# Performance work log

Measured on AMD Instinct MI355X. Metric: run time of the kernel, lower is better.

The kernel has to match this reference:

```python
import jax, jax.numpy as jnp
import numpy as np

NUM_LAYERS = 2
FEATURES = 128
INPUT_SIZE = 128
HIDDEN = 512
BATCH = 128
SEQ_LEN = 512
PRED_LEN = 128


def _uniform(key, shape, fan):
    bound = 1.0 / np.sqrt(fan)
    return jax.random.uniform(key, shape, jnp.float32, -bound, bound)


def setup_inputs() -> dict:
    key = jax.random.key(0)
    ks = jax.random.split(key, 14)
    inp = {}
    inp["x"] = jax.random.normal(ks[0], (BATCH, SEQ_LEN, FEATURES), jnp.float32)
    # encoder Linear(features -> input_size)
    inp["enc_w"] = _uniform(ks[1], (INPUT_SIZE, FEATURES), FEATURES)
    inp["enc_b"] = _uniform(ks[2], (INPUT_SIZE,), FEATURES)
    # decoder Linear(hidden -> input_size)
    inp["dec_w"] = _uniform(ks[3], (INPUT_SIZE, HIDDEN), HIDDEN)
    inp["dec_b"] = _uniform(ks[4], (INPUT_SIZE,), HIDDEN)
    # LSTM layer 0 (input_size -> hidden), gate order i,f,g,o as in PyTorch
    inp["wih0"] = _uniform(ks[5], (4 * HIDDEN, INPUT_SIZE), HIDDEN)
    inp["whh0"] = _uniform(ks[6], (4 * HIDDEN, HIDDEN), HIDDEN)
    inp["bih0"] = _uniform(ks[7], (4 * HIDDEN,), HIDDEN)
    inp["bhh0"] = _uniform(ks[8], (4 * HIDDEN,), HIDDEN)
    # LSTM layer 1 (hidden -> hidden)
    inp["wih1"] = _uniform(ks[9], (4 * HIDDEN, HIDDEN), HIDDEN)
    inp["whh1"] = _uniform(ks[10], (4 * HIDDEN, HIDDEN), HIDDEN)
    inp["bih1"] = _uniform(ks[11], (4 * HIDDEN,), HIDDEN)
    inp["bhh1"] = _uniform(ks[12], (4 * HIDDEN,), HIDDEN)
    inp["pred_len"] = PRED_LEN
    return inp


def _lstm_cell(h, c, inp, wih, whh, bih, bhh):
    g = inp @ wih.T + bih + h @ whh.T + bhh  # [B, 4H]
    i, f, gg, o = jnp.split(g, 4, axis=-1)
    c = jax.nn.sigmoid(f) * c + jax.nn.sigmoid(i) * jnp.tanh(gg)
    h = jax.nn.sigmoid(o) * jnp.tanh(c)
    return h, c


def reference(x, enc_w, enc_b, dec_w, dec_b, wih0, whh0, bih0, bhh0,
              wih1, whh1, bih1, bhh1, pred_len):
    B, S, Fdim = x.shape
    T = S + pred_len - 1
    # pad x to T steps; beyond S the input comes from the previous output
    x_pad = jnp.concatenate([x, jnp.zeros((B, pred_len - 1, Fdim), x.dtype)], axis=1)
    x_t = jnp.transpose(x_pad, (1, 0, 2))  # [T, B, F]

    def step(carry, xs):
        h0, c0, h1, c1, prev_out = carry
        xt, t = xs
        inp = jnp.where(t < S, xt, prev_out)
        e = inp @ enc_w.T + enc_b                    # encoder
        h0, c0 = _lstm_cell(h0, c0, e, wih0, whh0, bih0, bhh0)
        h1, c1 = _lstm_cell(h1, c1, h0, wih1, whh1, bih1, bhh1)
        out = h1 @ dec_w.T + dec_b                   # decoder
        return (h0, c0, h1, c1, out), out

    z = jnp.zeros((B, HIDDEN), x.dtype)
    init = (z, z, z, z, jnp.zeros((B, Fdim), x.dtype))
    _, outs = jax.lax.scan(step, init, (x_t, jnp.arange(T)))
    # keep steps idx >= S-1 (pred_len outputs), back to [B, pred_len, input_size]
    return jnp.transpose(outs[S - 1:], (1, 0, 2))
```

## Files before the change

### kernel.cpp

```cpp
#include <hip/hip_runtime.h>
#include <math.h>

#define HID 512
#define FEAT 128
#define SEQL 512
#define PREDL 128
#define NWG 256
#define HK 516
#define EK 132

typedef float v2f __attribute__((ext_vector_type(2)));

__device__ __forceinline__ float sigf_(float x) { return 1.0f / (1.0f + __expf(-x)); }
__device__ __forceinline__ float tanh_(float x) {
  float ax = fabsf(x);
  float e2 = __expf(-2.0f * ax);
  return copysignf((1.0f - e2) / (1.0f + e2), x);
}

__device__ __forceinline__ void stg_sc(float* p, float v) {
  __hip_atomic_store(p, v, __ATOMIC_RELAXED, __HIP_MEMORY_SCOPE_AGENT);
}

__device__ __forceinline__ void bar_arrive(int* __restrict__ bar, int grp,
                                           int phase, int tid, bool& last) {
  __syncthreads();
  if (tid == 0) {
    const int a = __hip_atomic_fetch_add(bar + grp * 32, 1, __ATOMIC_RELAXED,
                                         __HIP_MEMORY_SCOPE_AGENT);
    last = (a == 32 * phase - 1);
    if (last)
      __hip_atomic_store(bar + 512 + grp * 32, phase, __ATOMIC_RELAXED,
                         __HIP_MEMORY_SCOPE_AGENT);
  }
  asm volatile("" ::: "memory");
}
__device__ __forceinline__ void bar_wait(int* __restrict__ bar, int grp,
                                         int phase, int tid, bool last) {
  asm volatile("" ::: "memory");
  if (tid == 0 && !last) {
    while (__hip_atomic_load(bar + 512 + grp * 32, __ATOMIC_RELAXED,
                             __HIP_MEMORY_SCOPE_AGENT) < phase)
      __builtin_amdgcn_s_sleep(1);
  }
  __syncthreads();
}

__device__ __forceinline__ void stage_h2(float* __restrict__ dA,
                                         const float* __restrict__ sA,
                                         float* __restrict__ dB,
                                         const float* __restrict__ sB,
                                         int b0, int tid) {
  const int kb = tid >> 2;
  const int bq = (tid & 3) * 4;
  const float* a0 = sA + (size_t)kb * 128 + b0 + bq;
  const float* a1 = sA + ((size_t)kb + 128) * 128 + b0 + bq;
  const float* a2 = sA + ((size_t)kb + 256) * 128 + b0 + bq;
  const float* a3 = sA + ((size_t)kb + 384) * 128 + b0 + bq;
  const float* c0 = sB + (size_t)kb * 128 + b0 + bq;
  const float* c1 = sB + ((size_t)kb + 128) * 128 + b0 + bq;
  const float* c2 = sB + ((size_t)kb + 256) * 128 + b0 + bq;
  const float* c3 = sB + ((size_t)kb + 384) * 128 + b0 + bq;
  float4 r0, r1, r2, r3, q0, q1, q2, q3;
  asm volatile(
      "global_load_dwordx4 %0, %8, off sc0 sc1\n\t"
      "global_load_dwordx4 %1, %9, off sc0 sc1\n\t"
      "global_load_dwordx4 %2, %10, off sc0 sc1\n\t"
      "global_load_dwordx4 %3, %11, off sc0 sc1\n\t"
      "global_load_dwordx4 %4, %12, off sc0 sc1\n\t"
      "global_load_dwordx4 %5, %13, off sc0 sc1\n\t"
      "global_load_dwordx4 %6, %14, off sc0 sc1\n\t"
      "global_load_dwordx4 %7, %15, off sc0 sc1\n\t"
      "s_waitcnt vmcnt(0)"
      : "=&v"(r0), "=&v"(r1), "=&v"(r2), "=&v"(r3),
        "=&v"(q0), "=&v"(q1), "=&v"(q2), "=&v"(q3)
      : "v"(a0), "v"(a1), "v"(a2), "v"(a3),
        "v"(c0), "v"(c1), "v"(c2), "v"(c3)
      : "memory");
  dA[(bq + 0) * HK + kb] = r0.x; dA[(bq + 1) * HK + kb] = r0.y;
  dA[(bq + 2) * HK + kb] = r0.z; dA[(bq + 3) * HK + kb] = r0.w;
  dA[(bq + 0) * HK + kb + 128] = r1.x; dA[(bq + 1) * HK + kb + 128] = r1.y;
  dA[(bq + 2) * HK + kb + 128] = r1.z; dA[(bq + 3) * HK + kb + 128] = r1.w;
  dA[(bq + 0) * HK + kb + 256] = r2.x; dA[(bq + 1) * HK + kb + 256] = r2.y;
  dA[(bq + 2) * HK + kb + 256] = r2.z; dA[(bq + 3) * HK + kb + 256] = r2.w;
  dA[(bq + 0) * HK + kb + 384] = r3.x; dA[(bq + 1) * HK + kb + 384] = r3.y;
  dA[(bq + 2) * HK + kb + 384] = r3.z; dA[(bq + 3) * HK + kb + 384] = r3.w;
  dB[(bq + 0) * HK + kb] = q0.x; dB[(bq + 1) * HK + kb] = q0.y;
  dB[(bq + 2) * HK + kb] = q0.z; dB[(bq + 3) * HK + kb] = q0.w;
  dB[(bq + 0) * HK + kb + 128] = q1.x; dB[(bq + 1) * HK + kb + 128] = q1.y;
  dB[(bq + 2) * HK + kb + 128] = q1.z; dB[(bq + 3) * HK + kb + 128] = q1.w;
  dB[(bq + 0) * HK + kb + 256] = q2.x; dB[(bq + 1) * HK + kb + 256] = q2.y;
  dB[(bq + 2) * HK + kb + 256] = q2.z; dB[(bq + 3) * HK + kb + 256] = q2.w;
  dB[(bq + 0) * HK + kb + 384] = q3.x; dB[(bq + 1) * HK + kb + 384] = q3.y;
  dB[(bq + 2) * HK + kb + 384] = q3.z; dB[(bq + 3) * HK + kb + 384] = q3.w;
}
__device__ __forceinline__ void stage_h1t(float* __restrict__ dst,
                                          const float* __restrict__ src,
                                          int b0, int tid) {
  const int kb = tid >> 2;
  const int bq = (tid & 3) * 4;
  const float* p0 = src + (size_t)kb * 128 + b0 + bq;
  const float* p1 = src + ((size_t)kb + 128) * 128 + b0 + bq;
  const float* p2 = src + ((size_t)kb + 256) * 128 + b0 + bq;
  const float* p3 = src + ((size_t)kb + 384) * 128 + b0 + bq;
  float4 r0, r1, r2, r3;
  asm volatile(
      "global_load_dwordx4 %0, %4, off sc0 sc1\n\t"
      "global_load_dwordx4 %1, %5, off sc0 sc1\n\t"
      "global_load_dwordx4 %2, %6, off sc0 sc1\n\t"
      "global_load_dwordx4 %3, %7, off sc0 sc1\n\t"
      "s_waitcnt vmcnt(0)"
      : "=&v"(r0), "=&v"(r1), "=&v"(r2), "=&v"(r3)
      : "v"(p0), "v"(p1), "v"(p2), "v"(p3)
      : "memory");
  dst[(bq + 0) * HK + kb] = r0.x; dst[(bq + 1) * HK + kb] = r0.y;
  dst[(bq + 2) * HK + kb] = r0.z; dst[(bq + 3) * HK + kb] = r0.w;
  dst[(bq + 0) * HK + kb + 128] = r1.x; dst[(bq + 1) * HK + kb + 128] = r1.y;
  dst[(bq + 2) * HK + kb + 128] = r1.z; dst[(bq + 3) * HK + kb + 128] = r1.w;
  dst[(bq + 0) * HK + kb + 256] = r2.x; dst[(bq + 1) * HK + kb + 256] = r2.y;
  dst[(bq + 2) * HK + kb + 256] = r2.z; dst[(bq + 3) * HK + kb + 256] = r2.w;
  dst[(bq + 0) * HK + kb + 384] = r3.x; dst[(bq + 1) * HK + kb + 384] = r3.y;
  dst[(bq + 2) * HK + kb + 384] = r3.z; dst[(bq + 3) * HK + kb + 384] = r3.w;
}
__device__ __forceinline__ void stage_x(float* __restrict__ dst,
                                        const float* __restrict__ x, int t,
                                        int b0, int tid) {
  const int bb = tid >> 5;
  const int fq = (tid & 31) * 4;
  const float4 v =
      *(const float4*)(x + ((size_t)(b0 + bb) * SEQL + t) * FEAT + fq);
  *(float4*)(dst + bb * EK + fq) = v;
}

__device__ __forceinline__ void pkf(v2f& a01, v2f& a23, float4 w, float h) {
  v2f hh; hh[0] = h; hh[1] = h;
  v2f lo; lo[0] = w.x; lo[1] = w.y;
  v2f hi; hi[0] = w.z; hi[1] = w.w;
  a01 = __builtin_elementwise_fma(lo, hh, a01);
  a23 = __builtin_elementwise_fma(hi, hh, a23);
}
__device__ __forceinline__ void gemv_fused8(v2f& a01, v2f& a23,
                                            const float4* __restrict__ W8,
                                            size_t base,
                                            const float* __restrict__ rA,
                                            const float* __restrict__ rB,
                                            int k4b, int k4e) {
#pragma unroll 2
  for (int k4 = k4b; k4 < k4e; ++k4) {
    const float4 hA = *(const float4*)(rA + k4 * 4);
    const float4 hB = *(const float4*)(rB + k4 * 4);
    const size_t o = base + (size_t)k4 * 8;
    pkf(a01, a23, W8[o + 0], hA.x); pkf(a01, a23, W8[o + 1], hB.x);
    pkf(a01, a23, W8[o + 2], hA.y); pkf(a01, a23, W8[o + 3], hB.y);
    pkf(a01, a23, W8[o + 4], hA.z); pkf(a01, a23, W8[o + 5], hB.z);
    pkf(a01, a23, W8[o + 6], hA.w); pkf(a01, a23, W8[o + 7], hB.w);
  }
}
__device__ __forceinline__ void gemv_half8(v2f& a01, v2f& a23,
                                           const float4* __restrict__ W8,
                                           size_t base, int sel,
                                           const float* __restrict__ row,
                                           int nk4) {
#pragma unroll 4
  for (int k4 = 0; k4 < nk4; ++k4) {
    const float4 h = *(const float4*)(row + k4 * 4);
    const size_t o = base + (size_t)k4 * 8 + sel;
    pkf(a01, a23, W8[o + 0], h.x);
    pkf(a01, a23, W8[o + 2], h.y);
    pkf(a01, a23, W8[o + 4], h.z);
    pkf(a01, a23, W8[o + 6], h.w);
  }
}
__device__ __forceinline__ void gemv_p4(v2f& a01, v2f& a23,
                                        const float4* __restrict__ W4,
                                        size_t base,
                                        const float* __restrict__ row,
                                        int nk4) {
#pragma unroll 4
  for (int k4 = 0; k4 < nk4; ++k4) {
    const float4 h = *(const float4*)(row + k4 * 4);
    const size_t o = base + (size_t)k4 * 4;
    pkf(a01, a23, W4[o + 0], h.x);
    pkf(a01, a23, W4[o + 1], h.y);
    pkf(a01, a23, W4[o + 2], h.z);
    pkf(a01, a23, W4[o + 3], h.w);
  }
}

__device__ __forceinline__ void act_store(v2f a01, v2f a23, float& c_reg,
                                          float* __restrict__ HoutT,
                                          size_t cit) {
  const float ig = sigf_(a01[0]), fg = sigf_(a01[1]);
  const float gg = tanh_(a23[0]), og = sigf_(a23[1]);
  const float cn = fg * c_reg + ig * gg;
  c_reg = cn;
  stg_sc(HoutT + cit, og * tanh_(cn));
}

__global__ __launch_bounds__(512, 1) void k_persist(
    const float* __restrict__ x,
    const float* __restrict__ enc4, const float* __restrict__ enc_b,
    const float* __restrict__ wih04, const float* __restrict__ Wa8,
    const float* __restrict__ Wf8,
    const float* __restrict__ bih0, const float* __restrict__ bhh0,
    const float* __restrict__ bih1, const float* __restrict__ bhh1,
    const float* __restrict__ dec_w, const float* __restrict__ dec_b,
    const float* __restrict__ bcomp,
    float* __restrict__ h0A, float* __restrict__ h0B,
    float* __restrict__ h1A, float* __restrict__ h1B,
    int* __restrict__ bar, float* __restrict__ out) {
  __shared__ float s_h0[16 * HK];
  __shared__ float s_h1[16 * HK];
  __shared__ float s_x[16 * EK];
  __shared__ float s_e[16 * EK];
  __shared__ float s_red[1536];

  const int wg = blockIdx.x;
  const int tid = threadIdx.x;
  const int ut = (wg & 7) * 4 + ((wg >> 3) & 3);
  const int bt = wg >> 5;
  const int b0 = bt * 16;
  const int t8 = tid & 255;
  const int u = t8 >> 4, b = t8 & 15;
  const int ug = ut * 16 + u;
  const size_t cit = (size_t)ug * 128 + b0 + b;

  float* h0b[2] = {h0A, h0B};
  float* h1b[2] = {h1A, h1B};
  const float* sh0row = s_h0 + b * HK;
  const float* sh1row = s_h1 + b * HK;
  const float* serow = s_e + b * EK;

  const float4* W8a = (const float4*)Wa8;
  const float4* W8f = (const float4*)Wf8;
  const float4* W4i = (const float4*)wih04;
  const float4* W4e = (const float4*)enc4;
  const size_t baseG = (size_t)ug * 1024;
  const size_t baseI = (size_t)ug * 128;

  const float bt00 = bih0[ug] + bhh0[ug];
  const float bt01 = bih0[512 + ug] + bhh0[512 + ug];
  const float bt02 = bih0[1024 + ug] + bhh0[1024 + ug];
  const float bt03 = bih0[1536 + ug] + bhh0[1536 + ug];
  const float ba00 = bt00 + bcomp[ug];
  const float ba01 = bt01 + bcomp[512 + ug];
  const float ba02 = bt02 + bcomp[1024 + ug];
  const float ba03 = bt03 + bcomp[1536 + ug];
  const float b10 = bih1[ug] + bhh1[ug];
  const float b11 = bih1[512 + ug] + bhh1[512 + ug];
  const float b12 = bih1[1024 + ug] + bhh1[1024 + ug];
  const float b13 = bih1[1536 + ug] + bhh1[1536 + ug];

  const int eb = tid & 15;
  const int fb = tid >> 4;
  const size_t baseE = (size_t)fb * 128;
  const float eb0 = enc_b[fb * 4], eb1 = enc_b[fb * 4 + 1];
  const float eb2 = enc_b[fb * 4 + 2], eb3 = enc_b[fb * 4 + 3];
  const float* sxrow = s_x + eb * EK;

  const int djj = tid >> 7, dbb = (tid >> 3) & 15, dk8 = tid & 7;
  const int jd = (wg & 31) * 4 + djj;
  const float4* decr = (const float4*)(dec_w + (size_t)jd * HID);
  const float* dhrow = s_h1 + dbb * HK;

  float c_reg = 0.0f;
  int ph = 0;
  bool last = false;

  stage_x(s_x, x, 0, b0, tid);
  for (int t = 0; t < SEQL; ++t) {
    const float* h0in = h0b[(t + 1) & 1];
    float* h0out = h0b[t & 1];
    const float* h1in = h1b[t & 1];
    float* h1out = h1b[(t + 1) & 1];

    stage_h2(s_h0, h0in, s_h1, h1in, b0, tid);
    __syncthreads();

    {
      v2f a01; a01[0] = eb0; a01[1] = eb1;
      v2f a23; a23[0] = eb2; a23[1] = eb3;
      gemv_p4(a01, a23, W4e, baseE, sxrow, 32);
      *(float4*)(s_e + eb * EK + fb * 4) =
          make_float4(a01[0], a01[1], a23[0], a23[1]);
    }
    __syncthreads();

    if (tid < 256) {
      v2f a01; a01[0] = bt00; a01[1] = bt01;
      v2f a23; a23[0] = bt02; a23[1] = bt03;
      gemv_half8(a01, a23, W8a, baseG, 1, sh0row, 128);
      gemv_p4(a01, a23, W4i, baseI, serow, 32);
      act_store(a01, a23, c_reg, h0out, cit);
    } else if (t > 0) {
      v2f a01; a01[0] = b10; a01[1] = b11;
      v2f a23; a23[0] = b12; a23[1] = b13;
      gemv_fused8(a01, a23, W8f, baseG, sh0row, sh1row, 0, 128);
      act_store(a01, a23, c_reg, h1out, cit);
    }
    bar_arrive(bar, bt, ++ph, tid, last);
    if (t + 1 < SEQL) stage_x(s_x, x, t + 1, b0, tid);
    bar_wait(bar, bt, ph, tid, last);
  }

  stage_h2(s_h0, h0b[1], s_h1, h1b[0], b0, tid);
  __syncthreads();
  {
    const int own = (tid >= 256);
    v2f a01, a23;
    if (own) { a01[0] = b10; a01[1] = b11; a23[0] = b12; a23[1] = b13; }
    else { a01[0] = 0; a01[1] = 0; a23[0] = 0; a23[1] = 0; }
    const int kb4 = own ? 0 : 64;
    gemv_fused8(a01, a23, W8f, baseG, sh0row, sh1row, kb4, kb4 + 64);
    if (!own) {
      *(float4*)(s_red + t8 * 4) = make_float4(a01[0], a01[1], a23[0], a23[1]);
    }
    __syncthreads();
    if (own) {
      const float4 p = *(const float4*)(s_red + t8 * 4);
      a01[0] += p.x; a01[1] += p.y; a23[0] += p.z; a23[1] += p.w;
      act_store(a01, a23, c_reg, h1b[1], cit);
    }
  }
  bar_arrive(bar, bt, ++ph, tid, last);
  bar_wait(bar, bt, ph, tid, last);

  for (int t = SEQL; t < SEQL + PREDL - 1; ++t) {
    const float* h1prev = h1b[(t + 1) & 1];
    const float* h0prev = h0b[(t + 1) & 1];
    float* h0cur = h0b[t & 1];
    float* h1cur = h1b[t & 1];

    stage_h2(s_h1, h1prev, s_h0, h0prev, b0, tid);
    __syncthreads();
    {
      const int own = (tid < 256);
      v2f a01, a23;
      if (own) { a01[0] = ba00; a01[1] = ba01; a23[0] = ba02; a23[1] = ba03; }
      else { a01[0] = 0; a01[1] = 0; a23[0] = 0; a23[1] = 0; }
      const int kb4 = own ? 0 : 64;
      gemv_fused8(a01, a23, W8a, baseG, sh1row, sh0row, kb4, kb4 + 64);
      float dacc = 0.0f;
#pragma unroll 4
      for (int k4 = dk8 * 16; k4 < dk8 * 16 + 16; ++k4) {
        const float4 w = decr[k4];
        const float4 h = *(const float4*)(dhrow + k4 * 4);
        dacc += w.x * h.x + w.y * h.y + w.z * h.z + w.w * h.w;
      }
      s_red[1024 + tid] = dacc;
      if (!own)
        *(float4*)(s_red + t8 * 4) = make_float4(a01[0], a01[1], a23[0], a23[1]);
      __syncthreads();
      if (own) {
        const float4 p = *(const float4*)(s_red + t8 * 4);
        a01[0] += p.x; a01[1] += p.y; a23[0] += p.z; a23[1] += p.w;
        act_store(a01, a23, c_reg, h0cur, cit);
      }
      if (dk8 == 0) {
        float s = dec_b[jd];
#pragma unroll
        for (int i = 0; i < 8; ++i) s += s_red[1024 + tid + i];
        out[((size_t)(b0 + dbb) * PREDL + (t - SEQL)) * FEAT + jd] = s;
      }
    }
    bar_arrive(bar, bt, ++ph, tid, last);
    bar_wait(bar, bt, ph, tid, last);

    stage_h1t(s_h0, h0cur, b0, tid);
    __syncthreads();
    {
      const int own = (tid >= 256);
      v2f a01, a23;
      if (own) { a01[0] = b10; a01[1] = b11; a23[0] = b12; a23[1] = b13; }
      else { a01[0] = 0; a01[1] = 0; a23[0] = 0; a23[1] = 0; }
      const int kb4 = own ? 0 : 64;
      gemv_fused8(a01, a23, W8f, baseG, sh0row, sh1row, kb4, kb4 + 64);
      if (!own)
        *(float4*)(s_red + t8 * 4) = make_float4(a01[0], a01[1], a23[0], a23[1]);
      __syncthreads();
      if (own) {
        const float4 p = *(const float4*)(s_red + t8 * 4);
        a01[0] += p.x; a01[1] += p.y; a23[0] += p.z; a23[1] += p.w;
        act_store(a01, a23, c_reg, h1cur, cit);
      }
    }
    bar_arrive(bar, bt, ++ph, tid, last);
    bar_wait(bar, bt, ph, tid, last);
  }

  stage_h1t(s_h1, h1b[0], b0, tid);
  __syncthreads();
  {
    float dacc = 0.0f;
#pragma unroll 4
    for (int k4 = dk8 * 16; k4 < dk8 * 16 + 16; ++k4) {
      const float4 w = decr[k4];
      const float4 h = *(const float4*)(dhrow + k4 * 4);
      dacc += w.x * h.x + w.y * h.y + w.z * h.z + w.w * h.w;
    }
    s_red[1024 + tid] = dacc;
    __syncthreads();
    if (dk8 == 0) {
      float s = dec_b[jd];
#pragma unroll
      for (int i = 0; i < 8; ++i) s += s_red[1024 + tid + i];
      out[((size_t)(b0 + dbb) * PREDL + (PREDL - 1)) * FEAT + jd] = s;
    }
  }
}

__global__ void k_b1(const float* __restrict__ enc_w,
                     const float* __restrict__ dec_w, float* __restrict__ B1) {
  const int idx = blockIdx.x * 256 + threadIdx.x;
  const int j = idx >> 9, m = idx & 511;
  float acc = 0.0f;
  for (int k = 0; k < FEAT; ++k) acc += enc_w[j * FEAT + k] * dec_w[k * HID + m];
  B1[idx] = acc;
}
__global__ void k_te(const float* __restrict__ enc_w,
                     const float* __restrict__ enc_b,
                     const float* __restrict__ dec_b, float* __restrict__ te) {
  const int j = threadIdx.x;
  float acc = enc_b[j];
  for (int k = 0; k < FEAT; ++k) acc += dec_b[k] * enc_w[j * FEAT + k];
  te[j] = acc;
}
__global__ void k_bcomp(const float* __restrict__ wih0,
                        const float* __restrict__ te, float* __restrict__ bc) {
  const int n = blockIdx.x * 256 + threadIdx.x;
  float acc = 0.0f;
  for (int j = 0; j < FEAT; ++j) acc += wih0[n * FEAT + j] * te[j];
  bc[n] = acc;
}
__global__ void k_wa8(const float* __restrict__ wih0,
                      const float* __restrict__ B1,
                      const float* __restrict__ whh0, float* __restrict__ W) {
  const int idx = blockIdx.x * 256 + threadIdx.x;
  const int uu = idx >> 9, k = idx & 511;
  float c[4];
#pragma unroll
  for (int g = 0; g < 4; ++g) {
    const float* wr = wih0 + ((size_t)(g * 512 + uu)) * FEAT;
    float acc = 0.0f;
    for (int j = 0; j < FEAT; ++j) acc += wr[j] * B1[j * HID + k];
    c[g] = acc;
  }
  float4* o = (float4*)(W + ((size_t)(uu * 512 + k)) * 8);
  o[0] = make_float4(c[0], c[1], c[2], c[3]);
  o[1] = make_float4(whh0[((size_t)uu) * 512 + k],
                     whh0[((size_t)(512 + uu)) * 512 + k],
                     whh0[((size_t)(1024 + uu)) * 512 + k],
                     whh0[((size_t)(1536 + uu)) * 512 + k]);
}
__global__ void k_wf8(const float* __restrict__ wih1,
                      const float* __restrict__ whh1, float* __restrict__ W) {
  const int idx = blockIdx.x * 256 + threadIdx.x;
  const int uu = idx >> 9, k = idx & 511;
  float4* o = (float4*)(W + ((size_t)(uu * 512 + k)) * 8);
  o[0] = make_float4(wih1[((size_t)uu) * 512 + k],
                     wih1[((size_t)(512 + uu)) * 512 + k],
                     wih1[((size_t)(1024 + uu)) * 512 + k],
                     wih1[((size_t)(1536 + uu)) * 512 + k]);
  o[1] = make_float4(whh1[((size_t)uu) * 512 + k],
                     whh1[((size_t)(512 + uu)) * 512 + k],
                     whh1[((size_t)(1024 + uu)) * 512 + k],
                     whh1[((size_t)(1536 + uu)) * 512 + k]);
}
__global__ void k_wih04(const float* __restrict__ wih0, float* __restrict__ W) {
  const int idx = blockIdx.x * 256 + threadIdx.x;
  const int uu = idx >> 7, k = idx & 127;
  float4* o = (float4*)(W + ((size_t)idx) * 4);
  o[0] = make_float4(wih0[((size_t)uu) * FEAT + k],
                     wih0[((size_t)(512 + uu)) * FEAT + k],
                     wih0[((size_t)(1024 + uu)) * FEAT + k],
                     wih0[((size_t)(1536 + uu)) * FEAT + k]);
}
__global__ void k_enc4(const float* __restrict__ enc_w, float* __restrict__ W) {
  const int idx = blockIdx.x * 256 + threadIdx.x;
  const int fb = idx >> 7, k = idx & 127;
  float4* o = (float4*)(W + ((size_t)idx) * 4);
  o[0] = make_float4(enc_w[((size_t)(fb * 4 + 0)) * FEAT + k],
                     enc_w[((size_t)(fb * 4 + 1)) * FEAT + k],
                     enc_w[((size_t)(fb * 4 + 2)) * FEAT + k],
                     enc_w[((size_t)(fb * 4 + 3)) * FEAT + k]);
}

#define WS_H0A 0
#define WS_H0B 65536
#define WS_H1A 131072
#define WS_H1B 196608
#define WS_BAR 262144
#define WS_B1 263168
#define WS_TE 328704
#define WS_BCOMP 328832
#define WS_WIH04 330880
#define WS_ENC4 593024
#define WS_WA8 609408
#define WS_WF8 2706560

extern "C" void kernel_launch(void* const* d_in, const int* in_sizes, int n_in,
                              void* d_out, int out_size, void* d_ws,
                              size_t ws_size, hipStream_t stream) {
  const float* x     = (const float*)d_in[0];
  const float* enc_w = (const float*)d_in[1];
  const float* enc_b = (const float*)d_in[2];
  const float* dec_w = (const float*)d_in[3];
  const float* dec_b = (const float*)d_in[4];
  const float* wih0  = (const float*)d_in[5];
  const float* whh0  = (const float*)d_in[6];
  const float* bih0  = (const float*)d_in[7];
  const float* bhh0  = (const float*)d_in[8];
  const float* wih1  = (const float*)d_in[9];
  const float* whh1  = (const float*)d_in[10];
  const float* bih1  = (const float*)d_in[11];
  const float* bhh1  = (const float*)d_in[12];
  float* out = (float*)d_out;

  float* ws = (float*)d_ws;
  float* h0A = ws + WS_H0A;
  float* h0B = ws + WS_H0B;
  float* h1A = ws + WS_H1A;
  float* h1B = ws + WS_H1B;
  int* bar = (int*)(ws + WS_BAR);
  float* B1 = ws + WS_B1;
  float* te = ws + WS_TE;
  float* bcomp = ws + WS_BCOMP;
  float* wih04 = ws + WS_WIH04;
  float* enc4 = ws + WS_ENC4;
  float* Wa8 = ws + WS_WA8;
  float* Wf8 = ws + WS_WF8;

  hipMemsetAsync(ws, 0, (size_t)WS_B1 * sizeof(float), stream);

  k_b1<<<256, 256, 0, stream>>>(enc_w, dec_w, B1);
  k_te<<<1, 128, 0, stream>>>(enc_w, enc_b, dec_b, te);
  k_bcomp<<<8, 256, 0, stream>>>(wih0, te, bcomp);
  k_wa8<<<1024, 256, 0, stream>>>(wih0, B1, whh0, Wa8);
  k_wf8<<<1024, 256, 0, stream>>>(wih1, whh1, Wf8);
  k_wih04<<<256, 256, 0, stream>>>(wih0, wih04);
  k_enc4<<<16, 256, 0, stream>>>(enc_w, enc4);

  k_persist<<<NWG, 512, 0, stream>>>(
      x, enc4, enc_b, wih04, Wa8, Wf8, bih0, bhh0, bih1, bhh1,
      dec_w, dec_b, bcomp, h0A, h0B, h1A, h1B, bar, out);
}
```

Baseline: 37.38 ms.

## Double persistent workgroup to 1024 threads with split-K GEMV crews

Raises the persistent kernel from 512 to 1024 threads per workgroup and splits each gate GEMV's K range across two thread halves, reducing the partial sums through shared memory. Layer-1 tail steps use a four-way K split, and the decoder moves to its own thread crew with a repacked float4 weight layout so it runs alongside the layer-0 update. The encoder is re-tiled to two outputs per thread. The intent is to shorten the latency of each serial time step. In exchange it adds an extra __syncthreads per step, higher register pressure at 1024 threads, and shared-memory reductions.

```diff
diff --git a/kernel.cpp b/kernel.cpp
--- a/kernel.cpp
+++ b/kernel.cpp
@@ -17,6 +17,7 @@
   float e2 = __expf(-2.0f * ax);
   return copysignf((1.0f - e2) / (1.0f + e2), x);
 }
+__device__ __forceinline__ v2f mkv2(float a, float b) { v2f r; r[0] = a; r[1] = b; return r; }
 
 __device__ __forceinline__ void stg_sc(float* p, float v) {
   __hip_atomic_store(p, v, __ATOMIC_RELAXED, __HIP_MEMORY_SCOPE_AGENT);
@@ -46,59 +47,11 @@
   __syncthreads();
 }
 
-__device__ __forceinline__ void stage_h2(float* __restrict__ dA,
-                                         const float* __restrict__ sA,
-                                         float* __restrict__ dB,
-                                         const float* __restrict__ sB,
-                                         int b0, int tid) {
-  const int kb = tid >> 2;
-  const int bq = (tid & 3) * 4;
-  const float* a0 = sA + (size_t)kb * 128 + b0 + bq;
-  const float* a1 = sA + ((size_t)kb + 128) * 128 + b0 + bq;
-  const float* a2 = sA + ((size_t)kb + 256) * 128 + b0 + bq;
-  const float* a3 = sA + ((size_t)kb + 384) * 128 + b0 + bq;
-  const float* c0 = sB + (size_t)kb * 128 + b0 + bq;
-  const float* c1 = sB + ((size_t)kb + 128) * 128 + b0 + bq;
-  const float* c2 = sB + ((size_t)kb + 256) * 128 + b0 + bq;
-  const float* c3 = sB + ((size_t)kb + 384) * 128 + b0 + bq;
-  float4 r0, r1, r2, r3, q0, q1, q2, q3;
-  asm volatile(
-      "global_load_dwordx4 %0, %8, off sc0 sc1\n\t"
-      "global_load_dwordx4 %1, %9, off sc0 sc1\n\t"
-      "global_load_dwordx4 %2, %10, off sc0 sc1\n\t"
-      "global_load_dwordx4 %3, %11, off sc0 sc1\n\t"
-      "global_load_dwordx4 %4, %12, off sc0 sc1\n\t"
-      "global_load_dwordx4 %5, %13, off sc0 sc1\n\t"
-      "global_load_dwordx4 %6, %14, off sc0 sc1\n\t"
-      "global_load_dwordx4 %7, %15, off sc0 sc1\n\t"
-      "s_waitcnt vmcnt(0)"
-      : "=&v"(r0), "=&v"(r1), "=&v"(r2), "=&v"(r3),
-        "=&v"(q0), "=&v"(q1), "=&v"(q2), "=&v"(q3)
-      : "v"(a0), "v"(a1), "v"(a2), "v"(a3),
-        "v"(c0), "v"(c1), "v"(c2), "v"(c3)
-      : "memory");
-  dA[(bq + 0) * HK + kb] = r0.x; dA[(bq + 1) * HK + kb] = r0.y;
-  dA[(bq + 2) * HK + kb] = r0.z; dA[(bq + 3) * HK + kb] = r0.w;
-  dA[(bq + 0) * HK + kb + 128] = r1.x; dA[(bq + 1) * HK + kb + 128] = r1.y;
-  dA[(bq + 2) * HK + kb + 128] = r1.z; dA[(bq + 3) * HK + kb + 128] = r1.w;
-  dA[(bq + 0) * HK + kb + 256] = r2.x; dA[(bq + 1) * HK + kb + 256] = r2.y;
-  dA[(bq + 2) * HK + kb + 256] = r2.z; dA[(bq + 3) * HK + kb + 256] = r2.w;
-  dA[(bq + 0) * HK + kb + 384] = r3.x; dA[(bq + 1) * HK + kb + 384] = r3.y;
-  dA[(bq + 2) * HK + kb + 384] = r3.z; dA[(bq + 3) * HK + kb + 384] = r3.w;
-  dB[(bq + 0) * HK + kb] = q0.x; dB[(bq + 1) * HK + kb] = q0.y;
-  dB[(bq + 2) * HK + kb] = q0.z; dB[(bq + 3) * HK + kb] = q0.w;
-  dB[(bq + 0) * HK + kb + 128] = q1.x; dB[(bq + 1) * HK + kb + 128] = q1.y;
-  dB[(bq + 2) * HK + kb + 128] = q1.z; dB[(bq + 3) * HK + kb + 128] = q1.w;
-  dB[(bq + 0) * HK + kb + 256] = q2.x; dB[(bq + 1) * HK + kb + 256] = q2.y;
-  dB[(bq + 2) * HK + kb + 256] = q2.z; dB[(bq + 3) * HK + kb + 256] = q2.w;
-  dB[(bq + 0) * HK + kb + 384] = q3.x; dB[(bq + 1) * HK + kb + 384] = q3.y;
-  dB[(bq + 2) * HK + kb + 384] = q3.z; dB[(bq + 3) * HK + kb + 384] = q3.w;
-}
-__device__ __forceinline__ void stage_h1t(float* __restrict__ dst,
-                                          const float* __restrict__ src,
-                                          int b0, int tid) {
-  const int kb = tid >> 2;
-  const int bq = (tid & 3) * 4;
+__device__ __forceinline__ void stage4(float* __restrict__ dst,
+                                       const float* __restrict__ src,
+                                       int b0, int lane512) {
+  const int kb = lane512 >> 2;
+  const int bq = (lane512 & 3) * 4;
   const float* p0 = src + (size_t)kb * 128 + b0 + bq;
   const float* p1 = src + ((size_t)kb + 128) * 128 + b0 + bq;
   const float* p2 = src + ((size_t)kb + 256) * 128 + b0 + bq;
@@ -122,11 +75,11 @@
   dst[(bq + 0) * HK + kb + 384] = r3.x; dst[(bq + 1) * HK + kb + 384] = r3.y;
   dst[(bq + 2) * HK + kb + 384] = r3.z; dst[(bq + 3) * HK + kb + 384] = r3.w;
 }
-__device__ __forceinline__ void stage_x(float* __restrict__ dst,
-                                        const float* __restrict__ x, int t,
-                                        int b0, int tid) {
-  const int bb = tid >> 5;
-  const int fq = (tid & 31) * 4;
+__device__ __forceinline__ void stage_x1(float* __restrict__ dst,
+                                         const float* __restrict__ x, int t,
+                                         int b0, int lane512) {
+  const int bb = lane512 >> 5;
+  const int fq = (lane512 & 31) * 4;
   const float4 v =
       *(const float4*)(x + ((size_t)(b0 + bb) * SEQL + t) * FEAT + fq);
   *(float4*)(dst + bb * EK + fq) = v;
@@ -160,9 +113,9 @@
                                            const float4* __restrict__ W8,
                                            size_t base, int sel,
                                            const float* __restrict__ row,
-                                           int nk4) {
+                                           int k4b, int k4e) {
 #pragma unroll 4
-  for (int k4 = 0; k4 < nk4; ++k4) {
+  for (int k4 = k4b; k4 < k4e; ++k4) {
     const float4 h = *(const float4*)(row + k4 * 4);
     const size_t o = base + (size_t)k4 * 8 + sel;
     pkf(a01, a23, W8[o + 0], h.x);
@@ -175,9 +128,9 @@
                                         const float4* __restrict__ W4,
                                         size_t base,
                                         const float* __restrict__ row,
-                                        int nk4) {
+                                        int k4b, int k4e) {
 #pragma unroll 4
-  for (int k4 = 0; k4 < nk4; ++k4) {
+  for (int k4 = k4b; k4 < k4e; ++k4) {
     const float4 h = *(const float4*)(row + k4 * 4);
     const size_t o = base + (size_t)k4 * 4;
     pkf(a01, a23, W4[o + 0], h.x);
@@ -197,14 +150,14 @@
   stg_sc(HoutT + cit, og * tanh_(cn));
 }
 
-__global__ __launch_bounds__(512, 1) void k_persist(
+__global__ __launch_bounds__(1024, 1) void k_persist(
     const float* __restrict__ x,
-    const float* __restrict__ enc4, const float* __restrict__ enc_b,
+    const float* __restrict__ enc2, const float* __restrict__ enc_b,
     const float* __restrict__ wih04, const float* __restrict__ Wa8,
     const float* __restrict__ Wf8,
     const float* __restrict__ bih0, const float* __restrict__ bhh0,
     const float* __restrict__ bih1, const float* __restrict__ bhh1,
-    const float* __restrict__ dec_w, const float* __restrict__ dec_b,
+    const float* __restrict__ dec4, const float* __restrict__ dec_b,
     const float* __restrict__ bcomp,
     float* __restrict__ h0A, float* __restrict__ h0B,
     float* __restrict__ h1A, float* __restrict__ h1B,
@@ -213,17 +166,21 @@
   __shared__ float s_h1[16 * HK];
   __shared__ float s_x[16 * EK];
   __shared__ float s_e[16 * EK];
-  __shared__ float s_red[1536];
+  __shared__ float4 s_red4[768];
 
   const int wg = blockIdx.x;
   const int tid = threadIdx.x;
   const int ut = (wg & 7) * 4 + ((wg >> 3) & 3);
   const int bt = wg >> 5;
   const int b0 = bt * 16;
-  const int t8 = tid & 255;
-  const int u = t8 >> 4, b = t8 & 15;
+  const int o = tid & 255;
+  const int u = o >> 4, b = o & 15;
   const int ug = ut * 16 + u;
   const size_t cit = (size_t)ug * 128 + b0 + b;
+  const int crewB = tid >> 9;
+  const int khalf = (tid >> 8) & 1;
+  const int lane512 = tid & 511;
+  const int q4 = ((tid >> 8) + 2) & 3;
 
   float* h0b[2] = {h0A, h0B};
   float* h1b[2] = {h1A, h1B};
@@ -234,7 +191,6 @@
   const float4* W8a = (const float4*)Wa8;
   const float4* W8f = (const float4*)Wf8;
   const float4* W4i = (const float4*)wih04;
-  const float4* W4e = (const float4*)enc4;
   const size_t baseG = (size_t)ug * 1024;
   const size_t baseI = (size_t)ug * 128;
 
@@ -252,78 +208,100 @@
   const float b13 = bih1[1536 + ug] + bhh1[1536 + ug];
 
   const int eb = tid & 15;
-  const int fb = tid >> 4;
-  const size_t baseE = (size_t)fb * 128;
-  const float eb0 = enc_b[fb * 4], eb1 = enc_b[fb * 4 + 1];
-  const float eb2 = enc_b[fb * 4 + 2], eb3 = enc_b[fb * 4 + 3];
+  const int f2 = tid >> 4;
+  const float4* EF4 = (const float4*)enc2 + (size_t)f2 * 64;
+  const float encb0 = enc_b[f2 * 2], encb1 = enc_b[f2 * 2 + 1];
   const float* sxrow = s_x + eb * EK;
 
-  const int djj = tid >> 7, dbb = (tid >> 3) & 15, dk8 = tid & 7;
-  const int jd = (wg & 31) * 4 + djj;
-  const float4* decr = (const float4*)(dec_w + (size_t)jd * HID);
-  const float* dhrow = s_h1 + dbb * HK;
+  const int cb = tid & 511;
+  const int jq = cb >> 4, db = cb & 15;
+  const float4* D4 = (const float4*)dec4;
+  const size_t baseD = (size_t)jq * 512;
+  const float db0 = dec_b[jq * 4], db1 = dec_b[jq * 4 + 1];
+  const float db2 = dec_b[jq * 4 + 2], db3 = dec_b[jq * 4 + 3];
+  const float* dhrow = s_h1 + db * HK;
 
   float c_reg = 0.0f;
   int ph = 0;
-  bool last = false;
-
-  stage_x(s_x, x, 0, b0, tid);
+  bool lastf = false;
+
+  if (tid < 512) stage_x1(s_x, x, 0, b0, lane512);
   for (int t = 0; t < SEQL; ++t) {
     const float* h0in = h0b[(t + 1) & 1];
     float* h0out = h0b[t & 1];
     const float* h1in = h1b[t & 1];
     float* h1out = h1b[(t + 1) & 1];
 
-    stage_h2(s_h0, h0in, s_h1, h1in, b0, tid);
+    if (tid < 512) stage4(s_h0, h0in, b0, lane512);
+    else stage4(s_h1, h1in, b0, lane512);
     __syncthreads();
 
     {
-      v2f a01; a01[0] = eb0; a01[1] = eb1;
-      v2f a23; a23[0] = eb2; a23[1] = eb3;
-      gemv_p4(a01, a23, W4e, baseE, sxrow, 32);
-      *(float4*)(s_e + eb * EK + fb * 4) =
-          make_float4(a01[0], a01[1], a23[0], a23[1]);
-    }
-    __syncthreads();
-
-    if (tid < 256) {
-      v2f a01; a01[0] = bt00; a01[1] = bt01;
-      v2f a23; a23[0] = bt02; a23[1] = bt03;
-      gemv_half8(a01, a23, W8a, baseG, 1, sh0row, 128);
-      gemv_p4(a01, a23, W4i, baseI, serow, 32);
-      act_store(a01, a23, c_reg, h0out, cit);
-    } else if (t > 0) {
-      v2f a01; a01[0] = b10; a01[1] = b11;
-      v2f a23; a23[0] = b12; a23[1] = b13;
-      gemv_fused8(a01, a23, W8f, baseG, sh0row, sh1row, 0, 128);
-      act_store(a01, a23, c_reg, h1out, cit);
-    }
-    bar_arrive(bar, bt, ++ph, tid, last);
-    if (t + 1 < SEQL) stage_x(s_x, x, t + 1, b0, tid);
-    bar_wait(bar, bt, ph, tid, last);
-  }
-
-  stage_h2(s_h0, h0b[1], s_h1, h1b[0], b0, tid);
+      v2f acc = mkv2(encb0, encb1);
+#pragma unroll 8
+      for (int k2 = 0; k2 < 64; ++k2) {
+        const float4 w = EF4[k2];
+        const float hv0 = sxrow[2 * k2], hv1 = sxrow[2 * k2 + 1];
+        acc = __builtin_elementwise_fma(mkv2(w.x, w.y), mkv2(hv0, hv0), acc);
+        acc = __builtin_elementwise_fma(mkv2(w.z, w.w), mkv2(hv1, hv1), acc);
+      }
+      s_e[eb * EK + f2 * 2] = acc[0];
+      s_e[eb * EK + f2 * 2 + 1] = acc[1];
+    }
+    __syncthreads();
+
+    v2f a01, a23;
+    if (!crewB) {
+      if (!khalf) {
+        a01 = mkv2(bt00, bt01); a23 = mkv2(bt02, bt03);
+        gemv_half8(a01, a23, W8a, baseG, 1, sh0row, 0, 80);
+      } else {
+        a01 = mkv2(0.f, 0.f); a23 = mkv2(0.f, 0.f);
+        gemv_half8(a01, a23, W8a, baseG, 1, sh0row, 80, 128);
+        gemv_p4(a01, a23, W4i, baseI, serow, 0, 32);
+        s_red4[o] = make_float4(a01[0], a01[1], a23[0], a23[1]);
+      }
+    } else {
+      if (!khalf) {
+        a01 = mkv2(b10, b11); a23 = mkv2(b12, b13);
+        gemv_fused8(a01, a23, W8f, baseG, sh0row, sh1row, 0, 64);
+      } else {
+        a01 = mkv2(0.f, 0.f); a23 = mkv2(0.f, 0.f);
+        gemv_fused8(a01, a23, W8f, baseG, sh0row, sh1row, 64, 128);
+        s_red4[256 + o] = make_float4(a01[0], a01[1], a23[0], a23[1]);
+      }
+    }
+    __syncthreads();
+    if (!khalf) {
+      const float4 p = s_red4[(crewB ? 256 : 0) + o];
+      a01[0] += p.x; a01[1] += p.y; a23[0] += p.z; a23[1] += p.w;
+      if (!crewB) act_store(a01, a23, c_reg, h0out, cit);
+      else if (t > 0) act_store(a01, a23, c_reg, h1out, cit);
+    }
+    bar_arrive(bar, bt, ++ph, tid, lastf);
+    if (tid < 512 && t + 1 < SEQL) stage_x1(s_x, x, t + 1, b0, lane512);
+    bar_wait(bar, bt, ph, tid, lastf);
+  }
+
+  if (tid < 512) stage4(s_h0, h0b[1], b0, lane512);
+  else stage4(s_h1, h1b[0], b0, lane512);
   __syncthreads();
   {
-    const int own = (tid >= 256);
     v2f a01, a23;
-    if (own) { a01[0] = b10; a01[1] = b11; a23[0] = b12; a23[1] = b13; }
-    else { a01[0] = 0; a01[1] = 0; a23[0] = 0; a23[1] = 0; }
-    const int kb4 = own ? 0 : 64;
-    gemv_fused8(a01, a23, W8f, baseG, sh0row, sh1row, kb4, kb4 + 64);
-    if (!own) {
-      *(float4*)(s_red + t8 * 4) = make_float4(a01[0], a01[1], a23[0], a23[1]);
-    }
-    __syncthreads();
-    if (own) {
-      const float4 p = *(const float4*)(s_red + t8 * 4);
-      a01[0] += p.x; a01[1] += p.y; a23[0] += p.z; a23[1] += p.w;
+    if (q4 == 0) { a01 = mkv2(b10, b11); a23 = mkv2(b12, b13); }
+    else { a01 = mkv2(0.f, 0.f); a23 = mkv2(0.f, 0.f); }
+    gemv_fused8(a01, a23, W8f, baseG, sh0row, sh1row, q4 * 32, q4 * 32 + 32);
+    if (q4) s_red4[(q4 - 1) * 256 + o] = make_float4(a01[0], a01[1], a23[0], a23[1]);
+    __syncthreads();
+    if (q4 == 0) {
+      const float4 p0 = s_red4[o], p1 = s_red4[256 + o], p2 = s_red4[512 + o];
+      a01[0] += p0.x + p1.x + p2.x; a01[1] += p0.y + p1.y + p2.y;
+      a23[0] += p0.z + p1.z + p2.z; a23[1] += p0.w + p1.w + p2.w;
       act_store(a01, a23, c_reg, h1b[1], cit);
     }
   }
-  bar_arrive(bar, bt, ++ph, tid, last);
-  bar_wait(bar, bt, ph, tid, last);
+  bar_arrive(bar, bt, ++ph, tid, lastf);
+  bar_wait(bar, bt, ph, tid, lastf);
 
   for (int t = SEQL; t < SEQL + PREDL - 1; ++t) {
     const float* h1prev = h1b[(t + 1) & 1];
@@ -331,81 +309,58 @@
     float* h0cur = h0b[t & 1];
     float* h1cur = h1b[t & 1];
 
-    stage_h2(s_h1, h1prev, s_h0, h0prev, b0, tid);
+    if (tid < 512) stage4(s_h1, h1prev, b0, lane512);
+    else stage4(s_h0, h0prev, b0, lane512);
+    __syncthreads();
+    v2f a01, a23;
+    if (!crewB) {
+      if (!khalf) { a01 = mkv2(ba00, ba01); a23 = mkv2(ba02, ba03); }
+      else { a01 = mkv2(0.f, 0.f); a23 = mkv2(0.f, 0.f); }
+      gemv_fused8(a01, a23, W8a, baseG, sh1row, sh0row,
+                  khalf ? 64 : 0, khalf ? 128 : 64);
+      if (khalf) s_red4[o] = make_float4(a01[0], a01[1], a23[0], a23[1]);
+    } else {
+      v2f d01 = mkv2(db0, db1), d23 = mkv2(db2, db3);
+      gemv_p4(d01, d23, D4, baseD, dhrow, 0, 128);
+      *(float4*)(out + ((size_t)(b0 + db) * PREDL + (t - SEQL)) * FEAT + jq * 4) =
+          make_float4(d01[0], d01[1], d23[0], d23[1]);
+    }
+    __syncthreads();
+    if (!crewB && !khalf) {
+      const float4 p = s_red4[o];
+      a01[0] += p.x; a01[1] += p.y; a23[0] += p.z; a23[1] += p.w;
+      act_store(a01, a23, c_reg, h0cur, cit);
+    }
+    bar_arrive(bar, bt, ++ph, tid, lastf);
+    bar_wait(bar, bt, ph, tid, lastf);
+
+    if (tid < 512) stage4(s_h0, h0cur, b0, lane512);
     __syncthreads();
     {
-      const int own = (tid < 256);
-      v2f a01, a23;
-      if (own) { a01[0] = ba00; a01[1] = ba01; a23[0] = ba02; a23[1] = ba03; }
-      else { a01[0] = 0; a01[1] = 0; a23[0] = 0; a23[1] = 0; }
-      const int kb4 = own ? 0 : 64;
-      gemv_fused8(a01, a23, W8a, baseG, sh1row, sh0row, kb4, kb4 + 64);
-      float dacc = 0.0f;
-#pragma unroll 4
-      for (int k4 = dk8 * 16; k4 < dk8 * 16 + 16; ++k4) {
-        const float4 w = decr[k4];
-        const float4 h = *(const float4*)(dhrow + k4 * 4);
-        dacc += w.x * h.x + w.y * h.y + w.z * h.z + w.w * h.w;
+      v2f c01, c23;
+      if (q4 == 0) { c01 = mkv2(b10, b11); c23 = mkv2(b12, b13); }
+      else { c01 = mkv2(0.f, 0.f); c23 = mkv2(0.f, 0.f); }
+      gemv_fused8(c01, c23, W8f, baseG, sh0row, sh1row, q4 * 32, q4 * 32 + 32);
+      if (q4) s_red4[(q4 - 1) * 256 + o] = make_float4(c01[0], c01[1], c23[0], c23[1]);
+      __syncthreads();
+      if (q4 == 0) {
+        const float4 p0 = s_red4[o], p1 = s_red4[256 + o], p2 = s_red4[512 + o];
+        c01[0] += p0.x + p1.x + p2.x; c01[1] += p0.y + p1.y + p2.y;
+        c23[0] += p0.z + p1.z + p2.z; c23[1] += p0.w + p1.w + p2.w;
+        act_store(c01, c23, c_reg, h1cur, cit);
       }
-      s_red[1024 + tid] = dacc;
-      if (!own)
-        *(float4*)(s_red + t8 * 4) = make_float4(a01[0], a01[1], a23[0], a23[1]);
-      __syncthreads();
-      if (own) {
-        const float4 p = *(const float4*)(s_red + t8 * 4);
-        a01[0] += p.x; a01[1] += p.y; a23[0] += p.z; a23[1] += p.w;
-        act_store(a01, a23, c_reg, h0cur, cit);
-      }
-      if (dk8 == 0) {
-        float s = dec_b[jd];
-#pragma unroll
-        for (int i = 0; i < 8; ++i) s += s_red[1024 + tid + i];
-        out[((size_t)(b0 + dbb) * PREDL + (t - SEQL)) * FEAT + jd] = s;
-      }
-    }
-    bar_arrive(bar, bt, ++ph, tid, last);
-    bar_wait(bar, bt, ph, tid, last);
-
-    stage_h1t(s_h0, h0cur, b0, tid);
-    __syncthreads();
-    {
-      const int own = (tid >= 256);
-      v2f a01, a23;
-      if (own) { a01[0] = b10; a01[1] = b11; a23[0] = b12; a23[1] = b13; }
-      else { a01[0] = 0; a01[1] = 0; a23[0] = 0; a23[1] = 0; }
-      const int kb4 = own ? 0 : 64;
-      gemv_fused8(a01, a23, W8f, baseG, sh0row, sh1row, kb4, kb4 + 64);
-      if (!own)
-        *(float4*)(s_red + t8 * 4) = make_float4(a01[0], a01[1], a23[0], a23[1]);
-      __syncthreads();
-      if (own) {
-        const float4 p = *(const float4*)(s_red + t8 * 4);
-        a01[0] += p.x; a01[1] += p.y; a23[0] += p.z; a23[1] += p.w;
-        act_store(a01, a23, c_reg, h1cur, cit);
-      }
-    }
-    bar_arrive(bar, bt, ++ph, tid, last);
-    bar_wait(bar, bt, ph, tid, last);
-  }
-
-  stage_h1t(s_h1, h1b[0], b0, tid);
+    }
+    bar_arrive(bar, bt, ++ph, tid, lastf);
+    bar_wait(bar, bt, ph, tid, lastf);
+  }
+
+  if (tid < 512) stage4(s_h1, h1b[0], b0, lane512);
   __syncthreads();
-  {
-    float dacc = 0.0f;
-#pragma unroll 4
-    for (int k4 = dk8 * 16; k4 < dk8 * 16 + 16; ++k4) {
-      const float4 w = decr[k4];
-      const float4 h = *(const float4*)(dhrow + k4 * 4);
-      dacc += w.x * h.x + w.y * h.y + w.z * h.z + w.w * h.w;
-    }
-    s_red[1024 + tid] = dacc;
-    __syncthreads();
-    if (dk8 == 0) {
-      float s = dec_b[jd];
-#pragma unroll
-      for (int i = 0; i < 8; ++i) s += s_red[1024 + tid + i];
-      out[((size_t)(b0 + dbb) * PREDL + (PREDL - 1)) * FEAT + jd] = s;
-    }
+  if (crewB) {
+    v2f d01 = mkv2(db0, db1), d23 = mkv2(db2, db3);
+    gemv_p4(d01, d23, D4, baseD, dhrow, 0, 128);
+    *(float4*)(out + ((size_t)(b0 + db) * PREDL + (PREDL - 1)) * FEAT + jq * 4) =
+        make_float4(d01[0], d01[1], d23[0], d23[1]);
   }
 }
 
@@ -475,14 +430,20 @@
                      wih0[((size_t)(1024 + uu)) * FEAT + k],
                      wih0[((size_t)(1536 + uu)) * FEAT + k]);
 }
-__global__ void k_enc4(const float* __restrict__ enc_w, float* __restrict__ W) {
+__global__ void k_enc2(const float* __restrict__ enc_w, float* __restrict__ W) {
   const int idx = blockIdx.x * 256 + threadIdx.x;
-  const int fb = idx >> 7, k = idx & 127;
+  const int f2 = idx >> 7, k = idx & 127;
+  W[(size_t)idx * 2 + 0] = enc_w[((size_t)(f2 * 2 + 0)) * FEAT + k];
+  W[(size_t)idx * 2 + 1] = enc_w[((size_t)(f2 * 2 + 1)) * FEAT + k];
+}
+__global__ void k_dec4(const float* __restrict__ dec_w, float* __restrict__ W) {
+  const int idx = blockIdx.x * 256 + threadIdx.x;
+  const int jq = idx >> 9, k = idx & 511;
   float4* o = (float4*)(W + ((size_t)idx) * 4);
-  o[0] = make_float4(enc_w[((size_t)(fb * 4 + 0)) * FEAT + k],
-                     enc_w[((size_t)(fb * 4 + 1)) * FEAT + k],
-                     enc_w[((size_t)(fb * 4 + 2)) * FEAT + k],
-                     enc_w[((size_t)(fb * 4 + 3)) * FEAT + k]);
+  o[0] = make_float4(dec_w[((size_t)(jq * 4 + 0)) * HID + k],
+                     dec_w[((size_t)(jq * 4 + 1)) * HID + k],
+                     dec_w[((size_t)(jq * 4 + 2)) * HID + k],
+                     dec_w[((size_t)(jq * 4 + 3)) * HID + k]);
 }
 
 #define WS_H0A 0
@@ -494,9 +455,10 @@
 #define WS_TE 328704
 #define WS_BCOMP 328832
 #define WS_WIH04 330880
-#define WS_ENC4 593024
-#define WS_WA8 609408
-#define WS_WF8 2706560
+#define WS_ENC2 593024
+#define WS_DEC4 609408
+#define WS_WA8 674944
+#define WS_WF8 2772096
 
 extern "C" void kernel_launch(void* const* d_in, const int* in_sizes, int n_in,
                               void* d_out, int out_size, void* d_ws,
@@ -526,7 +488,8 @@
   float* te = ws + WS_TE;
   float* bcomp = ws + WS_BCOMP;
   float* wih04 = ws + WS_WIH04;
-  float* enc4 = ws + WS_ENC4;
+  float* enc2 = ws + WS_ENC2;
+  float* dec4 = ws + WS_DEC4;
   float* Wa8 = ws + WS_WA8;
   float* Wf8 = ws + WS_WF8;
 
@@ -538,9 +501,10 @@
   k_wa8<<<1024, 256, 0, stream>>>(wih0, B1, whh0, Wa8);
   k_wf8<<<1024, 256, 0, stream>>>(wih1, whh1, Wf8);
   k_wih04<<<256, 256, 0, stream>>>(wih0, wih04);
-  k_enc4<<<16, 256, 0, stream>>>(enc_w, enc4);
-
-  k_persist<<<NWG, 512, 0, stream>>>(
-      x, enc4, enc_b, wih04, Wa8, Wf8, bih0, bhh0, bih1, bhh1,
-      dec_w, dec_b, bcomp, h0A, h0B, h1A, h1B, bar, out);
-}
+  k_enc2<<<32, 256, 0, stream>>>(enc_w, enc2);
+  k_dec4<<<64, 256, 0, stream>>>(dec_w, dec4);
+
+  k_persist<<<NWG, 1024, 0, stream>>>(
+      x, enc2, enc_b, wih04, Wa8, Wf8, bih0, bhh0, bih1, bhh1,
+      dec4, dec_b, bcomp, h0A, h0B, h1A, h1B, bar, out);
+}
```

New measurement: 41.78 ms. 11.8% more time.
